# Kernel optimization log

Hardware: AMD Instinct MI355X
Metric: run time of the kernel (lower is better)

Reference implementation:

```python
import jax, jax.numpy as jnp
import numpy as np

N = 50000      # total nodes in batch
E = 800000     # edges (before self-loops)
F_IN = 64      # num_node_features
HID = 64       # hidden_channels
H = 4          # heads (hidden layers)
G = 512        # number of graphs
NEG_SLOPE = 0.2


def setup_inputs() -> dict:
    key = jax.random.key(0)
    ks = jax.random.split(key, 12)
    x = jax.random.normal(ks[0], (N, F_IN), dtype=jnp.float32)
    edge_index = jax.random.randint(ks[1], (2, E), 0, N, dtype=jnp.int32)
    # deterministic sorted graph assignment: all G segments non-empty
    batch = ((jnp.arange(N) * G) // N).astype(jnp.int32)

    def w(k, shape, fan_in):
        return (jax.random.normal(k, shape, jnp.float32) / np.sqrt(fan_in)).astype(jnp.float32)

    return {
        "x": x, "edge_index": edge_index, "batch": batch,
        # layer 0: in=F_IN, heads=4, concat -> out 256
        "W0": w(ks[2], (F_IN, H * HID), F_IN),
        "att_src0": w(ks[3], (H, HID), HID), "att_dst0": w(ks[4], (H, HID), HID),
        "b0": jnp.zeros((H * HID,), jnp.float32),
        # layer 1: in=256, heads=4, concat -> out 256
        "W1": w(ks[5], (H * HID, H * HID), H * HID),
        "att_src1": w(ks[6], (H, HID), HID), "att_dst1": w(ks[7], (H, HID), HID),
        "b1": jnp.zeros((H * HID,), jnp.float32),
        # layer 2: in=256, heads=1, concat=False -> out 64
        "W2": w(ks[8], (H * HID, 1 * HID), H * HID),
        "att_src2": w(ks[9], (1, HID), HID), "att_dst2": w(ks[10], (1, HID), HID),
        "b2": jnp.zeros((HID,), jnp.float32),
    }


def gat_layer(x, src, dst, W, att_src, att_dst, bias, concat):
    # PyG GATConv (eval mode, add_self_loops already applied to src/dst)
    n = x.shape[0]
    h, c = att_src.shape
    z = (x @ W).reshape(n, h, c)                       # [N,H,C]
    a_s = jnp.sum(z * att_src, axis=-1)                # [N,H]
    a_d = jnp.sum(z * att_dst, axis=-1)                # [N,H]
    e = jax.nn.leaky_relu(a_s[src] + a_d[dst], NEG_SLOPE)   # [E',H]
    # segment softmax over incoming edges of each target node
    e_max = jax.ops.segment_max(e, dst, num_segments=n)
    e_exp = jnp.exp(e - e_max[dst])
    denom = jax.ops.segment_sum(e_exp, dst, num_segments=n)
    alpha = e_exp / (denom[dst] + 1e-16)               # [E',H]
    msg = z[src] * alpha[:, :, None]                   # [E',H,C]
    out = jax.ops.segment_sum(msg, dst, num_segments=n)  # [N,H,C]
    out = out.reshape(n, h * c) if concat else out.mean(axis=1)
    return out + bias


def reference(x, edge_index, batch, W0, att_src0, att_dst0, b0,
              W1, att_src1, att_dst1, b1, W2, att_src2, att_dst2, b2):
    n = x.shape[0]
    loops = jnp.arange(n, dtype=edge_index.dtype)
    src = jnp.concatenate([edge_index[0], loops])
    dst = jnp.concatenate([edge_index[1], loops])
    h = gat_layer(x, src, dst, W0, att_src0, att_dst0, b0, concat=True)
    h = jax.nn.elu(h)
    h = gat_layer(h, src, dst, W1, att_src1, att_dst1, b1, concat=True)
    h = jax.nn.elu(h)
    h = gat_layer(h, src, dst, W2, att_src2, att_dst2, b2, concat=False)
    # global max pool over nodes of each graph -> [G, HID]
    return jax.ops.segment_max(h, batch, num_segments=G)
```

## Files before the change

### kernel.cpp

```cpp
#include <hip/hip_runtime.h>
#include <math.h>


typedef __attribute__((ext_vector_type(8))) short short8v;
typedef __attribute__((ext_vector_type(16))) float f32x16;

__device__ __forceinline__ float lrelu(float x) { return x > 0.f ? x : 0.2f * x; }

__device__ __forceinline__ unsigned short f2bf(float x) {
    unsigned u = __float_as_uint(x);
    return (unsigned short)((u + 0x7FFFu + ((u >> 16) & 1u)) >> 16);
}
__device__ __forceinline__ float bf2f(unsigned short h) {
    return __uint_as_float(((unsigned)h) << 16);
}
__device__ __forceinline__ float readlane_f(float v, int l) {
    return __uint_as_float((unsigned)__builtin_amdgcn_readlane((int)__float_as_uint(v), l));
}

__global__ void k_count(const int* __restrict__ dst, int E, int* __restrict__ deg) {
    int e = blockIdx.x * 256 + threadIdx.x;
    if (e < E) atomicAdd(&deg[dst[e]], 1);
}

__global__ __launch_bounds__(256) void k_scan1(const int* __restrict__ deg,
                                               int* __restrict__ incl,
                                               int* __restrict__ bsum, int N) {
    const int i = blockIdx.x * 256 + threadIdx.x;
    const int lane = threadIdx.x & 63;
    const int wv = threadIdx.x >> 6;
    int sc = (i < N) ? deg[i] + 1 : 0;
#pragma unroll
    for (int off = 1; off < 64; off <<= 1) {
        int t = __shfl_up(sc, off, 64);
        if (lane >= off) sc += t;
    }
    __shared__ int wsum[4];
    if (lane == 63) wsum[wv] = sc;
    __syncthreads();
    int woff = 0;
#pragma unroll
    for (int k = 0; k < 3; k++)
        if (wv > k) woff += wsum[k];
    sc += woff;
    if (i < N) incl[i] = sc;
    if (threadIdx.x == 255) bsum[blockIdx.x] = sc;
}

__global__ __launch_bounds__(1024) void k_scan2(int* __restrict__ bsum, int nb) {
    const int t = threadIdx.x;
    const int lane = t & 63;
    const int wv = t >> 6;
    int sc = (t < nb) ? bsum[t] : 0;
#pragma unroll
    for (int off = 1; off < 64; off <<= 1) {
        int u = __shfl_up(sc, off, 64);
        if (lane >= off) sc += u;
    }
    __shared__ int wsum[16];
    if (lane == 63) wsum[wv] = sc;
    __syncthreads();
    int woff = 0;
#pragma unroll
    for (int k = 0; k < 15; k++)
        if (wv > k) woff += wsum[k];
    sc += woff;
    if (t < nb) bsum[t] = sc;
}

__global__ void k_scan3(const int* __restrict__ deg, const int* __restrict__ incl,
                        const int* __restrict__ bsum, int* __restrict__ rowptr,
                        int* __restrict__ cursor, int N, int nb) {
    int i = blockIdx.x * 256 + threadIdx.x;
    if (i < N) {
        const int off = (blockIdx.x > 0) ? bsum[blockIdx.x - 1] : 0;
        const int excl = incl[i] + off - (deg[i] + 1);
        rowptr[i] = excl;
        cursor[i] = excl;
        if (i == N - 1) rowptr[N] = bsum[nb - 1];
    }
}

__global__ void k_scatter(const int* __restrict__ src, const int* __restrict__ dst, int E,
                          int N, int* __restrict__ cursor, int* __restrict__ col) {
    int e = blockIdx.x * 256 + threadIdx.x;
    if (e < E) {
        int d = dst[e];
        int p = atomicAdd(&cursor[d], 1);
        col[p] = src[e];
    } else if (e < E + N) {
        int n = e - E;
        int p = atomicAdd(&cursor[n], 1);
        col[p] = n;
    }
}

__global__ void k_setup(const float* __restrict__ W0, const float* __restrict__ W1,
                        const float* __restrict__ W2, const float* __restrict__ as0,
                        const float* __restrict__ ad0,
                        unsigned short* __restrict__ wt0h, unsigned short* __restrict__ wt0l,
                        unsigned short* __restrict__ wt1h, unsigned short* __restrict__ wt1l,
                        unsigned short* __restrict__ wt2h, unsigned short* __restrict__ wt2l,
                        float* __restrict__ vs0, float* __restrict__ vd0) {
    const int b = blockIdx.x;
    const int t = threadIdx.x;
    if (b < 64) {
        const int i = b * 256 + t;
        const int c = i / 64, k = i % 64;
        const float xw = W0[(size_t)k * 256 + c];
        const unsigned short h = f2bf(xw);
        wt0h[i] = h;
        wt0l[i] = f2bf(xw - bf2f(h));
    } else if (b < 320) {
        const int i = (b - 64) * 256 + t;
        const int c = i / 256, k = i % 256;
        const float xw = W1[(size_t)k * 256 + c];
        const unsigned short h = f2bf(xw);
        wt1h[i] = h;
        wt1l[i] = f2bf(xw - bf2f(h));
    } else if (b < 384) {
        const int i = (b - 320) * 256 + t;
        const int c = i / 256, k = i % 256;
        const float xw = W2[(size_t)k * 64 + c];
        const unsigned short h = f2bf(xw);
        wt2h[i] = h;
        wt2l[i] = f2bf(xw - bf2f(h));
    } else {
        const int k = t;
        if (k < 64) {
            for (int h = 0; h < 4; h++) {
                float s = 0.f, d = 0.f;
                for (int c = 0; c < 64; c++) {
                    float w = W0[(size_t)k * 256 + h * 64 + c];
                    s = fmaf(w, as0[h * 64 + c], s);
                    d = fmaf(w, ad0[h * 64 + c], d);
                }
                vs0[h * 64 + k] = s;
                vd0[h * 64 + k] = d;
            }
        }
    }
}

__global__ __launch_bounds__(256) void k_att0(
    const float* __restrict__ X, const float* __restrict__ vs, const float* __restrict__ vd,
    float* __restrict__ As, float* __restrict__ Ad, int N) {
    const int n = blockIdx.x * 4 + (threadIdx.x >> 6);
    const int lane = threadIdx.x & 63;
    if (n >= N) return;
    const float xv = X[(size_t)n * 64 + lane];
#pragma unroll
    for (int h = 0; h < 4; h++) {
        float ps = xv * vs[h * 64 + lane];
        float pd = xv * vd[h * 64 + lane];
#pragma unroll
        for (int off = 1; off < 64; off <<= 1) {
            ps += __shfl_xor(ps, off, 64);
            pd += __shfl_xor(pd, off, 64);
        }
        if (lane == 0) {
            As[(size_t)n * 4 + h] = ps;
            Ad[(size_t)n * 4 + h] = pd;
        }
    }
}

__global__ __launch_bounds__(256) void k_aggx(
    const float* __restrict__ X, const float* __restrict__ As, const float* __restrict__ Ad,
    const int* __restrict__ rowptr, const int* __restrict__ col,
    unsigned short* __restrict__ ohi, unsigned short* __restrict__ olo, int N) {
    __shared__ float wlds[4][64][4];
    const int wv = threadIdx.x >> 6;
    const int n = blockIdx.x * 4 + wv;
    const int lane = threadIdx.x & 63;
    if (n >= N) return;

    const int start = rowptr[n];
    const int total = rowptr[n + 1] - start;
    const int* __restrict__ cp = col + start;
    const float4 adn = *reinterpret_cast<const float4*>(Ad + (size_t)n * 4);

    float a0 = 0.f, a1 = 0.f, a2 = 0.f, a3 = 0.f;
    float d0 = 0.f, d1 = 0.f, d2 = 0.f, d3 = 0.f;

    for (int base = 0; base < total; base += 64) {
        const int cnt = min(64, total - base);
        const int i = base + lane;
        int s = 0;
        float4 w = make_float4(0.f, 0.f, 0.f, 0.f);
        if (i < total) {
            s = cp[i];
            const float4 av = *reinterpret_cast<const float4*>(As + (size_t)s * 4);
            w.x = __expf(lrelu(av.x + adn.x));
            w.y = __expf(lrelu(av.y + adn.y));
            w.z = __expf(lrelu(av.z + adn.z));
            w.w = __expf(lrelu(av.w + adn.w));
        }
        *reinterpret_cast<float4*>(&wlds[wv][lane][0]) = w;

        int jj = 0;
        for (; jj + 4 <= cnt; jj += 4) {
            int sb[4];
            float4 wj[4];
            float xv[4];
#pragma unroll
            for (int u = 0; u < 4; u++) {
                sb[u] = __builtin_amdgcn_readlane(s, jj + u);
                wj[u] = *reinterpret_cast<const float4*>(&wlds[wv][jj + u][0]);
            }
#pragma unroll
            for (int u = 0; u < 4; u++) xv[u] = X[(size_t)sb[u] * 64 + lane];
#pragma unroll
            for (int u = 0; u < 4; u++) {
                a0 = fmaf(wj[u].x, xv[u], a0);
                a1 = fmaf(wj[u].y, xv[u], a1);
                a2 = fmaf(wj[u].z, xv[u], a2);
                a3 = fmaf(wj[u].w, xv[u], a3);
                d0 += wj[u].x; d1 += wj[u].y; d2 += wj[u].z; d3 += wj[u].w;
            }
        }
        for (; jj < cnt; jj++) {
            const int s0 = __builtin_amdgcn_readlane(s, jj);
            const float4 wj = *reinterpret_cast<const float4*>(&wlds[wv][jj][0]);
            const float xv = X[(size_t)s0 * 64 + lane];
            a0 = fmaf(wj.x, xv, a0);
            a1 = fmaf(wj.y, xv, a1);
            a2 = fmaf(wj.z, xv, a2);
            a3 = fmaf(wj.w, xv, a3);
            d0 += wj.x; d1 += wj.y; d2 += wj.z; d3 += wj.w;
        }
    }

    const float o[4] = {a0 / (d0 + 1e-16f), a1 / (d1 + 1e-16f),
                        a2 / (d2 + 1e-16f), a3 / (d3 + 1e-16f)};
#pragma unroll
    for (int h = 0; h < 4; h++) {
        const unsigned short hb = f2bf(o[h]);
        ohi[(size_t)n * 256 + h * 64 + lane] = hb;
        olo[(size_t)n * 256 + h * 64 + lane] = f2bf(o[h] - bf2f(hb));
    }
}

__global__ __launch_bounds__(256) void k_gemm_pe(
    const unsigned short* __restrict__ Ahi, const unsigned short* __restrict__ Alo,
    const unsigned short* __restrict__ Bhi, const unsigned short* __restrict__ Blo,
    const float* __restrict__ bias, unsigned short* __restrict__ Ohi,
    unsigned short* __restrict__ Olo, int N) {
    constexpr int LD = 40, BM = 128, K = 64;
    __shared__ unsigned short sa[2][BM * LD];
    __shared__ unsigned short sb[2][64 * LD];

    const int tid = threadIdx.x;
    const int n0 = blockIdx.x * BM;
    const int hh = blockIdx.y;
    const int wid = tid >> 6, lane = tid & 63;

    const unsigned short* __restrict__ Ah = Ahi + hh * 64;
    const unsigned short* __restrict__ Al = Alo + hh * 64;
    const unsigned short* __restrict__ Bh = Bhi + hh * 64 * K;
    const unsigned short* __restrict__ Bl = Blo + hh * 64 * K;

    f32x16 acc[2];
#pragma unroll
    for (int n = 0; n < 2; n++)
#pragma unroll
        for (int i = 0; i < 16; i++) acc[n][i] = 0.f;

    const int srow = tid >> 2, schk = tid & 3;

    for (int kb = 0; kb < K; kb += 32) {
        __syncthreads();
#pragma unroll
        for (int rr = 0; rr < 2; rr++) {
            const int r = srow + rr * 64;
            const int row = n0 + r;
            short8v vh = {0, 0, 0, 0, 0, 0, 0, 0}, vl = {0, 0, 0, 0, 0, 0, 0, 0};
            if (row < N) {
                vh = *reinterpret_cast<const short8v*>(Ah + (size_t)row * 256 + kb + schk * 8);
                vl = *reinterpret_cast<const short8v*>(Al + (size_t)row * 256 + kb + schk * 8);
            }
            *reinterpret_cast<short8v*>(&sa[0][r * LD + schk * 8]) = vh;
            *reinterpret_cast<short8v*>(&sa[1][r * LD + schk * 8]) = vl;
        }
        {
            const short8v vh =
                *reinterpret_cast<const short8v*>(Bh + (size_t)srow * K + kb + schk * 8);
            const short8v vl =
                *reinterpret_cast<const short8v*>(Bl + (size_t)srow * K + kb + schk * 8);
            *reinterpret_cast<short8v*>(&sb[0][srow * LD + schk * 8]) = vh;
            *reinterpret_cast<short8v*>(&sb[1][srow * LD + schk * 8]) = vl;
        }
        __syncthreads();
#pragma unroll
        for (int ks = 0; ks < 2; ks++) {
            const int koff = ks * 16 + (lane >> 5) * 8;
            const int ar = wid * 32 + (lane & 31);
            const short8v ah = *reinterpret_cast<const short8v*>(&sa[0][ar * LD + koff]);
            const short8v al = *reinterpret_cast<const short8v*>(&sa[1][ar * LD + koff]);
            short8v bh[2], bl[2];
#pragma unroll
            for (int n = 0; n < 2; n++) {
                const int br = n * 32 + (lane & 31);
                bh[n] = *reinterpret_cast<const short8v*>(&sb[0][br * LD + koff]);
                bl[n] = *reinterpret_cast<const short8v*>(&sb[1][br * LD + koff]);
            }
#pragma unroll
            for (int n = 0; n < 2; n++) {
                acc[n] = __builtin_amdgcn_mfma_f32_32x32x16_bf16(ah, bh[n], acc[n], 0, 0, 0);
                acc[n] = __builtin_amdgcn_mfma_f32_32x32x16_bf16(ah, bl[n], acc[n], 0, 0, 0);
                acc[n] = __builtin_amdgcn_mfma_f32_32x32x16_bf16(al, bh[n], acc[n], 0, 0, 0);
            }
        }
    }

    const int rowb = n0 + wid * 32 + 4 * (lane >> 5);
#pragma unroll
    for (int n = 0; n < 2; n++) {
        const int c = (lane & 31) + n * 32;
        const float bv = bias[hh * 64 + c];
#pragma unroll
        for (int r = 0; r < 16; r++) {
            const int row = rowb + (r & 3) + 8 * (r >> 2);
            if (row < N) {
                float ov = acc[n][r] + bv;
                ov = (ov > 0.f) ? ov : expm1f(ov);
                const unsigned short hb = f2bf(ov);
                Ohi[(size_t)row * 256 + hh * 64 + c] = hb;
                Olo[(size_t)row * 256 + hh * 64 + c] = f2bf(ov - bf2f(hb));
            }
        }
    }
}

template <int K, int COLS, int BM, int BN, int WN>
__global__ __launch_bounds__(256) void k_gemm_z(
    const unsigned short* __restrict__ Ahi, const unsigned short* __restrict__ Alo,
    const unsigned short* __restrict__ Bhi, const unsigned short* __restrict__ Blo,
    const float* __restrict__ att_src, const float* __restrict__ att_dst,
    unsigned short* __restrict__ Zb, float* __restrict__ As, float* __restrict__ Ad, int N) {
    constexpr int LD = 40;
    constexpr int WAVES_N = BN / WN;
    constexpr int WAVES_M = 4 / WAVES_N;
    constexpr int WM = BM / WAVES_M;
    constexpr int MW = WM / 32, NW = WN / 32;
    constexpr int H = COLS / 64;
    __shared__ unsigned short sa[2][BM * LD];
    __shared__ unsigned short sb[2][BN * LD];

    const int tid = threadIdx.x;
    const int n0 = blockIdx.x * BM;
    const int c0 = blockIdx.y * BN;
    const int wid = tid >> 6, lane = tid & 63;
    const int wr = wid / WAVES_N, wc = wid % WAVES_N;

    f32x16 acc[MW][NW];
#pragma unroll
    for (int m = 0; m < MW; m++)
#pragma unroll
        for (int n = 0; n < NW; n++)
#pragma unroll
            for (int i = 0; i < 16; i++) acc[m][n][i] = 0.f;

    const int srow = tid >> 2, schk = tid & 3;

    for (int kb = 0; kb < K; kb += 32) {
        __syncthreads();
#pragma unroll
        for (int rr = 0; rr < BM / 64; rr++) {
            const int r = srow + rr * 64;
            const int row = n0 + r;
            short8v vh = {0, 0, 0, 0, 0, 0, 0, 0}, vl = {0, 0, 0, 0, 0, 0, 0, 0};
            if (row < N) {
                vh = *reinterpret_cast<const short8v*>(Ahi + (size_t)row * K + kb + schk * 8);
                vl = *reinterpret_cast<const short8v*>(Alo + (size_t)row * K + kb + schk * 8);
            }
            *reinterpret_cast<short8v*>(&sa[0][r * LD + schk * 8]) = vh;
            *reinterpret_cast<short8v*>(&sa[1][r * LD + schk * 8]) = vl;
        }
#pragma unroll
        for (int rr = 0; rr < BN / 64; rr++) {
            const int cc = srow + rr * 64;
            const short8v vh =
                *reinterpret_cast<const short8v*>(Bhi + (size_t)(c0 + cc) * K + kb + schk * 8);
            const short8v vl =
                *reinterpret_cast<const short8v*>(Blo + (size_t)(c0 + cc) * K + kb + schk * 8);
            *reinterpret_cast<short8v*>(&sb[0][cc * LD + schk * 8]) = vh;
            *reinterpret_cast<short8v*>(&sb[1][cc * LD + schk * 8]) = vl;
        }
        __syncthreads();
#pragma unroll
        for (int ks = 0; ks < 2; ks++) {
            const int koff = ks * 16 + (lane >> 5) * 8;
            short8v ah[MW], al[MW], bh[NW], bl[NW];
#pragma unroll
            for (int m = 0; m < MW; m++) {
                const int ar = wr * WM + m * 32 + (lane & 31);
                ah[m] = *reinterpret_cast<const short8v*>(&sa[0][ar * LD + koff]);
                al[m] = *reinterpret_cast<const short8v*>(&sa[1][ar * LD + koff]);
            }
#pragma unroll
            for (int n = 0; n < NW; n++) {
                const int br = wc * WN + n * 32 + (lane & 31);
                bh[n] = *reinterpret_cast<const short8v*>(&sb[0][br * LD + koff]);
                bl[n] = *reinterpret_cast<const short8v*>(&sb[1][br * LD + koff]);
            }
#pragma unroll
            for (int m = 0; m < MW; m++)
#pragma unroll
                for (int n = 0; n < NW; n++) {
                    acc[m][n] = __builtin_amdgcn_mfma_f32_32x32x16_bf16(ah[m], bh[n], acc[m][n], 0, 0, 0);
                    acc[m][n] = __builtin_amdgcn_mfma_f32_32x32x16_bf16(ah[m], bl[n], acc[m][n], 0, 0, 0);
                    acc[m][n] = __builtin_amdgcn_mfma_f32_32x32x16_bf16(al[m], bh[n], acc[m][n], 0, 0, 0);
                }
        }
    }

    const int colb = c0 + wc * WN + (lane & 31);
    const int rowb = n0 + wr * WM + 4 * (lane >> 5);
#pragma unroll
    for (int m = 0; m < MW; m++)
#pragma unroll
        for (int n = 0; n < NW; n++)
#pragma unroll
            for (int r = 0; r < 16; r++) {
                const int row = rowb + m * 32 + (r & 3) + 8 * (r >> 2);
                if (row < N) Zb[(size_t)row * COLS + colb + n * 32] = f2bf(acc[m][n][r]);
            }

    const int hh = (c0 + wc * WN) >> 6;
    float asv[NW], adv[NW];
#pragma unroll
    for (int n = 0; n < NW; n++) {
        asv[n] = att_src[colb + n * 32];
        adv[n] = att_dst[colb + n * 32];
    }
#pragma unroll
    for (int m = 0; m < MW; m++)
#pragma unroll
        for (int r = 0; r < 16; r++) {
            const int row = rowb + m * 32 + (r & 3) + 8 * (r >> 2);
            float ps = 0.f, pd = 0.f;
#pragma unroll
            for (int n = 0; n < NW; n++) {
                ps = fmaf(acc[m][n][r], asv[n], ps);
                pd = fmaf(acc[m][n][r], adv[n], pd);
            }
#pragma unroll
            for (int off = 1; off < 32; off <<= 1) {
                ps += __shfl_xor(ps, off, 64);
                pd += __shfl_xor(pd, off, 64);
            }
            if ((lane & 31) == 0 && row < N) {
                As[(size_t)row * H + hh] = ps;
                Ad[(size_t)row * H + hh] = pd;
            }
        }
}

__device__ __forceinline__ unsigned fenc(float f) {
    unsigned u = __float_as_uint(f);
    return (u & 0x80000000u) ? ~u : (u | 0x80000000u);
}

__global__ __launch_bounds__(256) void k_agg4(
    const unsigned short* __restrict__ Zb, const float* __restrict__ As,
    const float* __restrict__ Ad, const int* __restrict__ rowptr,
    const int* __restrict__ col, const float* __restrict__ bias,
    unsigned short* __restrict__ ohi, unsigned short* __restrict__ olo, int N) {
    __shared__ float wlds[4][64][4];
    const int wv = threadIdx.x >> 6;
    const int n = blockIdx.x * 4 + wv;
    const int lane = threadIdx.x & 63;
    if (n >= N) return;
    const int h = lane >> 4;

    const int start = rowptr[n];
    const int total = rowptr[n + 1] - start;
    const int* __restrict__ cp = col + start;
    const float4 adn = *reinterpret_cast<const float4*>(Ad + (size_t)n * 4);
    const unsigned short* __restrict__ Zl = Zb + lane * 4;

    float a0 = 0.f, a1 = 0.f, a2 = 0.f, a3 = 0.f;
    float den = 0.f;

    for (int base = 0; base < total; base += 64) {
        const int cnt = min(64, total - base);
        const int i = base + lane;
        int s = 0;
        float4 w = make_float4(0.f, 0.f, 0.f, 0.f);
        if (i < total) {
            s = cp[i];
            const float4 av = *reinterpret_cast<const float4*>(As + (size_t)s * 4);
            w.x = __expf(lrelu(av.x + adn.x));
            w.y = __expf(lrelu(av.y + adn.y));
            w.z = __expf(lrelu(av.z + adn.z));
            w.w = __expf(lrelu(av.w + adn.w));
        }
        *reinterpret_cast<float4*>(&wlds[wv][lane][0]) = w;

        int jj = 0;
        for (; jj + 8 <= cnt; jj += 8) {
            int sb[8];
            float ws[8];
            ushort4 zb[8];
#pragma unroll
            for (int u = 0; u < 8; u++) {
                sb[u] = __builtin_amdgcn_readlane(s, jj + u);
                ws[u] = wlds[wv][jj + u][h];
            }
#pragma unroll
            for (int u = 0; u < 8; u++)
                zb[u] = *reinterpret_cast<const ushort4*>(Zl + (size_t)sb[u] * 256);
#pragma unroll
            for (int u = 0; u < 8; u++) {
                a0 = fmaf(ws[u], bf2f(zb[u].x), a0);
                a1 = fmaf(ws[u], bf2f(zb[u].y), a1);
                a2 = fmaf(ws[u], bf2f(zb[u].z), a2);
                a3 = fmaf(ws[u], bf2f(zb[u].w), a3);
                den += ws[u];
            }
        }
        for (; jj + 4 <= cnt; jj += 4) {
            int sb[4];
            float ws[4];
            ushort4 zb[4];
#pragma unroll
            for (int u = 0; u < 4; u++) {
                sb[u] = __builtin_amdgcn_readlane(s, jj + u);
                ws[u] = wlds[wv][jj + u][h];
            }
#pragma unroll
            for (int u = 0; u < 4; u++)
                zb[u] = *reinterpret_cast<const ushort4*>(Zl + (size_t)sb[u] * 256);
#pragma unroll
            for (int u = 0; u < 4; u++) {
                a0 = fmaf(ws[u], bf2f(zb[u].x), a0);
                a1 = fmaf(ws[u], bf2f(zb[u].y), a1);
                a2 = fmaf(ws[u], bf2f(zb[u].z), a2);
                a3 = fmaf(ws[u], bf2f(zb[u].w), a3);
                den += ws[u];
            }
        }
        for (; jj < cnt; jj++) {
            const int s0 = __builtin_amdgcn_readlane(s, jj);
            const float ws = wlds[wv][jj][h];
            const ushort4 zb = *reinterpret_cast<const ushort4*>(Zl + (size_t)s0 * 256);
            a0 = fmaf(ws, bf2f(zb.x), a0);
            a1 = fmaf(ws, bf2f(zb.y), a1);
            a2 = fmaf(ws, bf2f(zb.z), a2);
            a3 = fmaf(ws, bf2f(zb.w), a3);
            den += ws;
        }
    }

    const float inv = 1.f / (den + 1e-16f);
    float o[4] = {a0, a1, a2, a3};
#pragma unroll
    for (int j = 0; j < 4; j++) {
        float ov = o[j] * inv + bias[lane * 4 + j];
        ov = (ov > 0.f) ? ov : expm1f(ov);
        o[j] = ov;
    }
    const unsigned short b0 = f2bf(o[0]), b1 = f2bf(o[1]), b2 = f2bf(o[2]), b3 = f2bf(o[3]);
    const ushort4 vh = make_ushort4(b0, b1, b2, b3);
    const ushort4 vl = make_ushort4(f2bf(o[0] - bf2f(b0)), f2bf(o[1] - bf2f(b1)),
                                    f2bf(o[2] - bf2f(b2)), f2bf(o[3] - bf2f(b3)));
    *reinterpret_cast<ushort4*>(ohi + (size_t)n * 256 + lane * 4) = vh;
    *reinterpret_cast<ushort4*>(olo + (size_t)n * 256 + lane * 4) = vl;
}

__global__ __launch_bounds__(256) void k_agg1(
    const unsigned short* __restrict__ Zb, const float* __restrict__ As,
    const float* __restrict__ Ad, const int* __restrict__ rowptr,
    const int* __restrict__ col, const float* __restrict__ bias,
    const int* __restrict__ batch, unsigned* __restrict__ enc, int N) {
    const int n = blockIdx.x * 4 + (threadIdx.x >> 6);
    const int lane = threadIdx.x & 63;
    if (n >= N) return;

    const int start = rowptr[n];
    const int total = rowptr[n + 1] - start;
    const int* __restrict__ cp = col + start;
    const float adn = Ad[n];

    float acc = 0.f, denom = 0.f;

    for (int base = 0; base < total; base += 64) {
        const int cnt = min(64, total - base);
        const int i = base + lane;
        int s = 0;
        float w = 0.f;
        if (i < total) {
            s = cp[i];
            w = __expf(lrelu(As[s] + adn));
        }

        int jj = 0;
        for (; jj + 8 <= cnt; jj += 8) {
            int sb[8];
            float wb[8], zb[8];
#pragma unroll
            for (int u = 0; u < 8; u++) {
                sb[u] = __builtin_amdgcn_readlane(s, jj + u);
                wb[u] = readlane_f(w, jj + u);
            }
#pragma unroll
            for (int u = 0; u < 8; u++) zb[u] = bf2f(Zb[(size_t)sb[u] * 64 + lane]);
#pragma unroll
            for (int u = 0; u < 8; u++) {
                acc = fmaf(wb[u], zb[u], acc);
                denom += wb[u];
            }
        }
        for (; jj < cnt; jj++) {
            const int s0 = __builtin_amdgcn_readlane(s, jj);
            const float w0 = readlane_f(w, jj);
            acc = fmaf(w0, bf2f(Zb[(size_t)s0 * 64 + lane]), acc);
            denom += w0;
        }
    }

    const float ov = acc / (denom + 1e-16f) + bias[lane];
    const int g = batch[n];
    atomicMax(&enc[g * 64 + lane], fenc(ov));
}

__global__ void k_decode(const unsigned* __restrict__ enc, float* __restrict__ out, int M) {
    int id = blockIdx.x * 256 + threadIdx.x;
    if (id < M) {
        unsigned e = enc[id];
        unsigned u = (e & 0x80000000u) ? (e & 0x7FFFFFFFu) : ~e;
        out[id] = __uint_as_float(u);
    }
}

extern "C" void kernel_launch(void* const* d_in, const int* in_sizes, int n_in,
                              void* d_out, int out_size, void* d_ws, size_t ws_size,
                              hipStream_t stream) {
    const float* x = (const float*)d_in[0];
    const int* edge_index = (const int*)d_in[1];
    const int* batch = (const int*)d_in[2];
    const float* W0 = (const float*)d_in[3];
    const float* as0 = (const float*)d_in[4];
    const float* ad0 = (const float*)d_in[5];
    const float* b0 = (const float*)d_in[6];
    const float* W1 = (const float*)d_in[7];
    const float* as1 = (const float*)d_in[8];
    const float* ad1 = (const float*)d_in[9];
    const float* b1 = (const float*)d_in[10];
    const float* W2 = (const float*)d_in[11];
    const float* as2 = (const float*)d_in[12];
    const float* ad2 = (const float*)d_in[13];
    const float* b2 = (const float*)d_in[14];

    const int N = in_sizes[0] / 64;
    const int E = in_sizes[1] / 2;
    const int G = out_size / 64;
    const int Et = E + N;

    const int* srcs = edge_index;
    const int* dsts = edge_index + E;

    char* p = (char*)d_ws;
    auto alloc = [&](size_t bytes) {
        void* r = (void*)p;
        p += (bytes + 255) & ~(size_t)255;
        return r;
    };
    unsigned short* Zb = (unsigned short*)alloc((size_t)N * 256 * 2);
    unsigned short* Hbhi = (unsigned short*)alloc((size_t)N * 256 * 2);
    unsigned short* Hblo = (unsigned short*)alloc((size_t)N * 256 * 2);
    unsigned short* Axhi = (unsigned short*)alloc((size_t)N * 256 * 2);
    unsigned short* Axlo = (unsigned short*)alloc((size_t)N * 256 * 2);
    float* As = (float*)alloc((size_t)N * 4 * 4);
    float* Ad = (float*)alloc((size_t)N * 4 * 4);
    int* deg = (int*)alloc((size_t)N * 4);
    int* incl = (int*)alloc((size_t)N * 4);
    int* bsum = (int*)alloc(1024 * 4);
    int* rowptr = (int*)alloc((size_t)(N + 1) * 4);
    int* cursor = (int*)alloc((size_t)N * 4);
    int* col = (int*)alloc((size_t)Et * 4);
    unsigned short* wt0h = (unsigned short*)alloc(256 * 64 * 2);
    unsigned short* wt0l = (unsigned short*)alloc(256 * 64 * 2);
    unsigned short* wt1h = (unsigned short*)alloc(256 * 256 * 2);
    unsigned short* wt1l = (unsigned short*)alloc(256 * 256 * 2);
    unsigned short* wt2h = (unsigned short*)alloc(64 * 256 * 2);
    unsigned short* wt2l = (unsigned short*)alloc(64 * 256 * 2);
    float* vs0 = (float*)alloc(4 * 64 * 4);
    float* vd0 = (float*)alloc(4 * 64 * 4);
    unsigned* enc = (unsigned*)alloc((size_t)G * 64 * 4);

    hipMemsetAsync(deg, 0, (size_t)N * 4, stream);
    hipMemsetAsync(enc, 0, (size_t)G * 64 * 4, stream);

    const int eb = (E + 255) / 256;
    const int nb = (N + 255) / 256;
    const int ab = (N + 3) / 4;
    const int gm = (N + 127) / 128;

    k_count<<<eb, 256, 0, stream>>>(dsts, E, deg);
    k_scan1<<<nb, 256, 0, stream>>>(deg, incl, bsum, N);
    k_scan2<<<1, 1024, 0, stream>>>(bsum, nb);
    k_scan3<<<nb, 256, 0, stream>>>(deg, incl, bsum, rowptr, cursor, N, nb);
    k_scatter<<<(Et + 255) / 256, 256, 0, stream>>>(srcs, dsts, E, N, cursor, col);

    k_setup<<<385, 256, 0, stream>>>(W0, W1, W2, as0, ad0, wt0h, wt0l, wt1h, wt1l,
                                     wt2h, wt2l, vs0, vd0);

    k_att0<<<ab, 256, 0, stream>>>(x, vs0, vd0, As, Ad, N);
    k_aggx<<<ab, 256, 0, stream>>>(x, As, Ad, rowptr, col, Axhi, Axlo, N);
    k_gemm_pe<<<dim3(gm, 4), 256, 0, stream>>>(Axhi, Axlo, wt0h, wt0l, b0, Hbhi, Hblo, N);

    k_gemm_z<256, 256, 128, 128, 64><<<dim3(gm, 2), 256, 0, stream>>>(
        Hbhi, Hblo, wt1h, wt1l, as1, ad1, Zb, As, Ad, N);
    k_agg4<<<ab, 256, 0, stream>>>(Zb, As, Ad, rowptr, col, b1, Hbhi, Hblo, N);

    k_gemm_z<256, 64, 128, 64, 64><<<dim3(gm, 1), 256, 0, stream>>>(
        Hbhi, Hblo, wt2h, wt2l, as2, ad2, Zb, As, Ad, N);
    k_agg1<<<ab, 256, 0, stream>>>(Zb, As, Ad, rowptr, col, b2, batch, enc, N);
    k_decode<<<(G * 64 + 255) / 256, 256, 0, stream>>>(enc, (float*)d_out, G * 64);
}
```

Measured before the change: 390.8 us.

## Drop bf16 lo-split for hidden activations and gather x as bf16

Hidden activations are now stored as a single bf16 array instead of a hi/lo bf16 pair. The lo-part MFMA in the layer-1/2 GEMMs and the lo loads and stores in the aggregation kernels are removed. The input features are converted to bf16 once in k_att0, so the first-layer gather reads half the bytes. Softmax denominators are now accumulated per lane and reduced with a wave shuffle instead of being summed inside the inner loop. The aim is less memory traffic and fewer MFMAs, paid for with reduced precision of the activations and the layer-1/2 GEMM inputs.

```diff
diff --git a/kernel.cpp b/kernel.cpp
--- a/kernel.cpp
+++ b/kernel.cpp
@@ -144,11 +144,12 @@
 
 __global__ __launch_bounds__(256) void k_att0(
     const float* __restrict__ X, const float* __restrict__ vs, const float* __restrict__ vd,
-    float* __restrict__ As, float* __restrict__ Ad, int N) {
+    float* __restrict__ As, float* __restrict__ Ad, unsigned short* __restrict__ xb, int N) {
     const int n = blockIdx.x * 4 + (threadIdx.x >> 6);
     const int lane = threadIdx.x & 63;
     if (n >= N) return;
     const float xv = X[(size_t)n * 64 + lane];
+    xb[(size_t)n * 64 + lane] = f2bf(xv);
 #pragma unroll
     for (int h = 0; h < 4; h++) {
         float ps = xv * vs[h * 64 + lane];
@@ -166,9 +167,10 @@
 }
 
 __global__ __launch_bounds__(256) void k_aggx(
-    const float* __restrict__ X, const float* __restrict__ As, const float* __restrict__ Ad,
-    const int* __restrict__ rowptr, const int* __restrict__ col,
-    unsigned short* __restrict__ ohi, unsigned short* __restrict__ olo, int N) {
+    const unsigned short* __restrict__ Xb, const float* __restrict__ As,
+    const float* __restrict__ Ad, const int* __restrict__ rowptr,
+    const int* __restrict__ col, unsigned short* __restrict__ ohi,
+    unsigned short* __restrict__ olo, int N) {
     __shared__ float wlds[4][64][4];
     const int wv = threadIdx.x >> 6;
     const int n = blockIdx.x * 4 + wv;
@@ -181,7 +183,7 @@
     const float4 adn = *reinterpret_cast<const float4*>(Ad + (size_t)n * 4);
 
     float a0 = 0.f, a1 = 0.f, a2 = 0.f, a3 = 0.f;
-    float d0 = 0.f, d1 = 0.f, d2 = 0.f, d3 = 0.f;
+    float4 dv = make_float4(0.f, 0.f, 0.f, 0.f);
 
     for (int base = 0; base < total; base += 64) {
         const int cnt = min(64, total - base);
@@ -196,6 +198,7 @@
             w.z = __expf(lrelu(av.z + adn.z));
             w.w = __expf(lrelu(av.w + adn.w));
         }
+        dv.x += w.x; dv.y += w.y; dv.z += w.z; dv.w += w.w;
         *reinterpret_cast<float4*>(&wlds[wv][lane][0]) = w;
 
         int jj = 0;
@@ -209,30 +212,36 @@
                 wj[u] = *reinterpret_cast<const float4*>(&wlds[wv][jj + u][0]);
             }
 #pragma unroll
-            for (int u = 0; u < 4; u++) xv[u] = X[(size_t)sb[u] * 64 + lane];
+            for (int u = 0; u < 4; u++) xv[u] = bf2f(Xb[(size_t)sb[u] * 64 + lane]);
 #pragma unroll
             for (int u = 0; u < 4; u++) {
                 a0 = fmaf(wj[u].x, xv[u], a0);
                 a1 = fmaf(wj[u].y, xv[u], a1);
                 a2 = fmaf(wj[u].z, xv[u], a2);
                 a3 = fmaf(wj[u].w, xv[u], a3);
-                d0 += wj[u].x; d1 += wj[u].y; d2 += wj[u].z; d3 += wj[u].w;
             }
         }
         for (; jj < cnt; jj++) {
             const int s0 = __builtin_amdgcn_readlane(s, jj);
             const float4 wj = *reinterpret_cast<const float4*>(&wlds[wv][jj][0]);
-            const float xv = X[(size_t)s0 * 64 + lane];
+            const float xv = bf2f(Xb[(size_t)s0 * 64 + lane]);
             a0 = fmaf(wj.x, xv, a0);
             a1 = fmaf(wj.y, xv, a1);
             a2 = fmaf(wj.z, xv, a2);
             a3 = fmaf(wj.w, xv, a3);
-            d0 += wj.x; d1 += wj.y; d2 += wj.z; d3 += wj.w;
-        }
-    }
-
-    const float o[4] = {a0 / (d0 + 1e-16f), a1 / (d1 + 1e-16f),
-                        a2 / (d2 + 1e-16f), a3 / (d3 + 1e-16f)};
+        }
+    }
+
+#pragma unroll
+    for (int off = 1; off < 64; off <<= 1) {
+        dv.x += __shfl_xor(dv.x, off, 64);
+        dv.y += __shfl_xor(dv.y, off, 64);
+        dv.z += __shfl_xor(dv.z, off, 64);
+        dv.w += __shfl_xor(dv.w, off, 64);
+    }
+
+    const float o[4] = {a0 / (dv.x + 1e-16f), a1 / (dv.y + 1e-16f),
+                        a2 / (dv.z + 1e-16f), a3 / (dv.w + 1e-16f)};
 #pragma unroll
     for (int h = 0; h < 4; h++) {
         const unsigned short hb = f2bf(o[h]);
@@ -244,8 +253,7 @@
 __global__ __launch_bounds__(256) void k_gemm_pe(
     const unsigned short* __restrict__ Ahi, const unsigned short* __restrict__ Alo,
     const unsigned short* __restrict__ Bhi, const unsigned short* __restrict__ Blo,
-    const float* __restrict__ bias, unsigned short* __restrict__ Ohi,
-    unsigned short* __restrict__ Olo, int N) {
+    const float* __restrict__ bias, unsigned short* __restrict__ Ohi, int N) {
     constexpr int LD = 40, BM = 128, K = 64;
     __shared__ unsigned short sa[2][BM * LD];
     __shared__ unsigned short sb[2][64 * LD];
@@ -324,9 +332,7 @@
             if (row < N) {
                 float ov = acc[n][r] + bv;
                 ov = (ov > 0.f) ? ov : expm1f(ov);
-                const unsigned short hb = f2bf(ov);
-                Ohi[(size_t)row * 256 + hh * 64 + c] = hb;
-                Olo[(size_t)row * 256 + hh * 64 + c] = f2bf(ov - bf2f(hb));
+                Ohi[(size_t)row * 256 + hh * 64 + c] = f2bf(ov);
             }
         }
     }
@@ -334,7 +340,7 @@
 
 template <int K, int COLS, int BM, int BN, int WN>
 __global__ __launch_bounds__(256) void k_gemm_z(
-    const unsigned short* __restrict__ Ahi, const unsigned short* __restrict__ Alo,
+    const unsigned short* __restrict__ Ahi,
     const unsigned short* __restrict__ Bhi, const unsigned short* __restrict__ Blo,
     const float* __restrict__ att_src, const float* __restrict__ att_dst,
     unsigned short* __restrict__ Zb, float* __restrict__ As, float* __restrict__ Ad, int N) {
@@ -344,7 +350,7 @@
     constexpr int WM = BM / WAVES_M;
     constexpr int MW = WM / 32, NW = WN / 32;
     constexpr int H = COLS / 64;
-    __shared__ unsigned short sa[2][BM * LD];
+    __shared__ unsigned short sa[BM * LD];
     __shared__ unsigned short sb[2][BN * LD];
 
     const int tid = threadIdx.x;
@@ -369,13 +375,10 @@
         for (int rr = 0; rr < BM / 64; rr++) {
             const int r = srow + rr * 64;
             const int row = n0 + r;
-            short8v vh = {0, 0, 0, 0, 0, 0, 0, 0}, vl = {0, 0, 0, 0, 0, 0, 0, 0};
-            if (row < N) {
+            short8v vh = {0, 0, 0, 0, 0, 0, 0, 0};
+            if (row < N)
                 vh = *reinterpret_cast<const short8v*>(Ahi + (size_t)row * K + kb + schk * 8);
-                vl = *reinterpret_cast<const short8v*>(Alo + (size_t)row * K + kb + schk * 8);
-            }
-            *reinterpret_cast<short8v*>(&sa[0][r * LD + schk * 8]) = vh;
-            *reinterpret_cast<short8v*>(&sa[1][r * LD + schk * 8]) = vl;
+            *reinterpret_cast<short8v*>(&sa[r * LD + schk * 8]) = vh;
         }
 #pragma unroll
         for (int rr = 0; rr < BN / 64; rr++) {
@@ -391,12 +394,11 @@
 #pragma unroll
         for (int ks = 0; ks < 2; ks++) {
             const int koff = ks * 16 + (lane >> 5) * 8;
-            short8v ah[MW], al[MW], bh[NW], bl[NW];
+            short8v ah[MW], bh[NW], bl[NW];
 #pragma unroll
             for (int m = 0; m < MW; m++) {
                 const int ar = wr * WM + m * 32 + (lane & 31);
-                ah[m] = *reinterpret_cast<const short8v*>(&sa[0][ar * LD + koff]);
-                al[m] = *reinterpret_cast<const short8v*>(&sa[1][ar * LD + koff]);
+                ah[m] = *reinterpret_cast<const short8v*>(&sa[ar * LD + koff]);
             }
 #pragma unroll
             for (int n = 0; n < NW; n++) {
@@ -410,7 +412,6 @@
                 for (int n = 0; n < NW; n++) {
                     acc[m][n] = __builtin_amdgcn_mfma_f32_32x32x16_bf16(ah[m], bh[n], acc[m][n], 0, 0, 0);
                     acc[m][n] = __builtin_amdgcn_mfma_f32_32x32x16_bf16(ah[m], bl[n], acc[m][n], 0, 0, 0);
-                    acc[m][n] = __builtin_amdgcn_mfma_f32_32x32x16_bf16(al[m], bh[n], acc[m][n], 0, 0, 0);
                 }
         }
     }
@@ -466,7 +467,7 @@
     const unsigned short* __restrict__ Zb, const float* __restrict__ As,
     const float* __restrict__ Ad, const int* __restrict__ rowptr,
     const int* __restrict__ col, const float* __restrict__ bias,
-    unsigned short* __restrict__ ohi, unsigned short* __restrict__ olo, int N) {
+    unsigned short* __restrict__ ohi, int N) {
     __shared__ float wlds[4][64][4];
     const int wv = threadIdx.x >> 6;
     const int n = blockIdx.x * 4 + wv;
@@ -481,7 +482,7 @@
     const unsigned short* __restrict__ Zl = Zb + lane * 4;
 
     float a0 = 0.f, a1 = 0.f, a2 = 0.f, a3 = 0.f;
-    float den = 0.f;
+    float4 dv = make_float4(0.f, 0.f, 0.f, 0.f);
 
     for (int base = 0; base < total; base += 64) {
         const int cnt = min(64, total - base);
@@ -496,6 +497,7 @@
             w.z = __expf(lrelu(av.z + adn.z));
             w.w = __expf(lrelu(av.w + adn.w));
         }
+        dv.x += w.x; dv.y += w.y; dv.z += w.z; dv.w += w.w;
         *reinterpret_cast<float4*>(&wlds[wv][lane][0]) = w;
 
         int jj = 0;
@@ -517,7 +519,6 @@
                 a1 = fmaf(ws[u], bf2f(zb[u].y), a1);
                 a2 = fmaf(ws[u], bf2f(zb[u].z), a2);
                 a3 = fmaf(ws[u], bf2f(zb[u].w), a3);
-                den += ws[u];
             }
         }
         for (; jj + 4 <= cnt; jj += 4) {
@@ -538,7 +539,6 @@
                 a1 = fmaf(ws[u], bf2f(zb[u].y), a1);
                 a2 = fmaf(ws[u], bf2f(zb[u].z), a2);
                 a3 = fmaf(ws[u], bf2f(zb[u].w), a3);
-                den += ws[u];
             }
         }
         for (; jj < cnt; jj++) {
@@ -549,24 +549,26 @@
             a1 = fmaf(ws, bf2f(zb.y), a1);
             a2 = fmaf(ws, bf2f(zb.z), a2);
             a3 = fmaf(ws, bf2f(zb.w), a3);
-            den += ws;
-        }
-    }
-
+        }
+    }
+
+#pragma unroll
+    for (int off = 1; off < 64; off <<= 1) {
+        dv.x += __shfl_xor(dv.x, off, 64);
+        dv.y += __shfl_xor(dv.y, off, 64);
+        dv.z += __shfl_xor(dv.z, off, 64);
+        dv.w += __shfl_xor(dv.w, off, 64);
+    }
+    const float den = (h == 0) ? dv.x : (h == 1) ? dv.y : (h == 2) ? dv.z : dv.w;
     const float inv = 1.f / (den + 1e-16f);
     float o[4] = {a0, a1, a2, a3};
 #pragma unroll
     for (int j = 0; j < 4; j++) {
         float ov = o[j] * inv + bias[lane * 4 + j];
-        ov = (ov > 0.f) ? ov : expm1f(ov);
-        o[j] = ov;
-    }
-    const unsigned short b0 = f2bf(o[0]), b1 = f2bf(o[1]), b2 = f2bf(o[2]), b3 = f2bf(o[3]);
-    const ushort4 vh = make_ushort4(b0, b1, b2, b3);
-    const ushort4 vl = make_ushort4(f2bf(o[0] - bf2f(b0)), f2bf(o[1] - bf2f(b1)),
-                                    f2bf(o[2] - bf2f(b2)), f2bf(o[3] - bf2f(b3)));
+        o[j] = (ov > 0.f) ? ov : expm1f(ov);
+    }
+    const ushort4 vh = make_ushort4(f2bf(o[0]), f2bf(o[1]), f2bf(o[2]), f2bf(o[3]));
     *reinterpret_cast<ushort4*>(ohi + (size_t)n * 256 + lane * 4) = vh;
-    *reinterpret_cast<ushort4*>(olo + (size_t)n * 256 + lane * 4) = vl;
 }
 
 __global__ __launch_bounds__(256) void k_agg1(
@@ -594,6 +596,7 @@
             s = cp[i];
             w = __expf(lrelu(As[s] + adn));
         }
+        denom += w;
 
         int jj = 0;
         for (; jj + 8 <= cnt; jj += 8) {
@@ -607,18 +610,17 @@
 #pragma unroll
             for (int u = 0; u < 8; u++) zb[u] = bf2f(Zb[(size_t)sb[u] * 64 + lane]);
 #pragma unroll
-            for (int u = 0; u < 8; u++) {
-                acc = fmaf(wb[u], zb[u], acc);
-                denom += wb[u];
-            }
+            for (int u = 0; u < 8; u++) acc = fmaf(wb[u], zb[u], acc);
         }
         for (; jj < cnt; jj++) {
             const int s0 = __builtin_amdgcn_readlane(s, jj);
             const float w0 = readlane_f(w, jj);
             acc = fmaf(w0, bf2f(Zb[(size_t)s0 * 64 + lane]), acc);
-            denom += w0;
-        }
-    }
+        }
+    }
+
+#pragma unroll
+    for (int off = 1; off < 64; off <<= 1) denom += __shfl_xor(denom, off, 64);
 
     const float ov = acc / (denom + 1e-16f) + bias[lane];
     const int g = batch[n];
@@ -668,8 +670,8 @@
         return r;
     };
     unsigned short* Zb = (unsigned short*)alloc((size_t)N * 256 * 2);
-    unsigned short* Hbhi = (unsigned short*)alloc((size_t)N * 256 * 2);
-    unsigned short* Hblo = (unsigned short*)alloc((size_t)N * 256 * 2);
+    unsigned short* Hb = (unsigned short*)alloc((size_t)N * 256 * 2);
+    unsigned short* xb = (unsigned short*)alloc((size_t)N * 64 * 2);
     unsigned short* Axhi = (unsigned short*)alloc((size_t)N * 256 * 2);
     unsigned short* Axlo = (unsigned short*)alloc((size_t)N * 256 * 2);
     float* As = (float*)alloc((size_t)N * 4 * 4);
@@ -707,16 +709,16 @@
     k_setup<<<385, 256, 0, stream>>>(W0, W1, W2, as0, ad0, wt0h, wt0l, wt1h, wt1l,
                                      wt2h, wt2l, vs0, vd0);
 
-    k_att0<<<ab, 256, 0, stream>>>(x, vs0, vd0, As, Ad, N);
-    k_aggx<<<ab, 256, 0, stream>>>(x, As, Ad, rowptr, col, Axhi, Axlo, N);
-    k_gemm_pe<<<dim3(gm, 4), 256, 0, stream>>>(Axhi, Axlo, wt0h, wt0l, b0, Hbhi, Hblo, N);
+    k_att0<<<ab, 256, 0, stream>>>(x, vs0, vd0, As, Ad, xb, N);
+    k_aggx<<<ab, 256, 0, stream>>>(xb, As, Ad, rowptr, col, Axhi, Axlo, N);
+    k_gemm_pe<<<dim3(gm, 4), 256, 0, stream>>>(Axhi, Axlo, wt0h, wt0l, b0, Hb, N);
 
     k_gemm_z<256, 256, 128, 128, 64><<<dim3(gm, 2), 256, 0, stream>>>(
-        Hbhi, Hblo, wt1h, wt1l, as1, ad1, Zb, As, Ad, N);
-    k_agg4<<<ab, 256, 0, stream>>>(Zb, As, Ad, rowptr, col, b1, Hbhi, Hblo, N);
+        Hb, wt1h, wt1l, as1, ad1, Zb, As, Ad, N);
+    k_agg4<<<ab, 256, 0, stream>>>(Zb, As, Ad, rowptr, col, b1, Hb, N);
 
     k_gemm_z<256, 64, 128, 64, 64><<<dim3(gm, 1), 256, 0, stream>>>(
-        Hbhi, Hblo, wt2h, wt2l, as2, ad2, Zb, As, Ad, N);
+        Hb, wt2h, wt2l, as2, ad2, Zb, As, Ad, N);
     k_agg1<<<ab, 256, 0, stream>>>(Zb, As, Ad, rowptr, col, b2, batch, enc, N);
     k_decode<<<(G * 64 + 255) / 256, 256, 0, stream>>>(enc, (float*)d_out, G * 64);
 }
```

Result: faster. 369.2 us (-5.5%).
